# Performance work log

Measured on AMD Instinct MI355X. Metric: run time of the kernel, lower is better.

The kernel has to match this reference:

```python
import jax, jax.numpy as jnp
import numpy as np

B, T, C = 4, 2048, 1024
N_HEAD = 16
HEAD = C // N_HEAD

def setup_inputs() -> dict:
    key = jax.random.key(0)
    k1, k2, k3 = jax.random.split(key, 3)
    x = jax.random.normal(k1, (B, T, C), dtype=jnp.float32)
    w_attn = jax.random.normal(k2, (C, 3 * C), dtype=jnp.float32) * (1.0 / np.sqrt(C))
    w_proj = jax.random.normal(k3, (C, C), dtype=jnp.float32) * (1.0 / np.sqrt(C))
    return {"x": x, "w_attn": w_attn, "w_proj": w_proj}

def reference(x, w_attn, w_proj):
    b, t, c = x.shape
    qkv = x @ w_attn  # [B,T,3C]
    q, k, v = jnp.split(qkv, 3, axis=-1)
    # [B,T,C] -> [B,H,T,D]
    def heads(z):
        return z.reshape(b, t, N_HEAD, HEAD).transpose(0, 2, 1, 3)
    q, k, v = heads(q), heads(k), heads(v)
    scale = 1.0 / np.sqrt(HEAD)
    att = jnp.einsum('bhqd,bhkd->bhqk', q, k) * scale  # [B,H,T,T]
    causal = jnp.tril(jnp.ones((t, t), dtype=bool))
    att = jnp.where(causal[None, None], att, -jnp.inf)
    att = jax.nn.softmax(att, axis=-1)
    y = jnp.einsum('bhqk,bhkd->bhqd', att, v)  # [B,H,T,D]
    y = y.transpose(0, 2, 1, 3).reshape(b, t, c)
    return y @ w_proj
```

## Files before the change

kernel.cpp:

```cpp
#include <hip/hip_runtime.h>
#include <hip/hip_bf16.h>


typedef __attribute__((ext_vector_type(8))) short bf16x8;
typedef __attribute__((ext_vector_type(4))) float f32x4;

#define T_DIM 2048
#define NHEAD 16
#define HDIM  64

__device__ __forceinline__ unsigned short f2bf(float f) {
    union { float f; unsigned int u; } v; v.f = f;
    unsigned int r = v.u + 0x7fffu + ((v.u >> 16) & 1u);
    return (unsigned short)(r >> 16);
}

__device__ __forceinline__ void gload_lds16(const void* g, void* l) {
    __builtin_amdgcn_global_load_lds(
        (const __attribute__((address_space(1))) void*)g,
        (__attribute__((address_space(3))) void*)l,
        16, 0, 0);
}

__global__ void cvt_bf16_k(const float* __restrict__ src, unsigned short* __restrict__ dst, int n) {
    int i = (blockIdx.x * blockDim.x + threadIdx.x) * 4;
    if (i < n) {
        float4 v = *(const float4*)(src + i);
        ushort4 o; o.x = f2bf(v.x); o.y = f2bf(v.y); o.z = f2bf(v.z); o.w = f2bf(v.w);
        *(ushort4*)(dst + i) = o;
    }
}

__global__ void transpose_wb_k(const float* __restrict__ src, unsigned short* __restrict__ dst,
                               int R, int Cc) {
    __shared__ float tile[32][33];
    int c0 = blockIdx.x * 32, r0 = blockIdx.y * 32;
    int tx = threadIdx.x & 31, ty = threadIdx.x >> 5;
    #pragma unroll
    for (int i = 0; i < 32; i += 8)
        tile[ty + i][tx] = src[(size_t)(r0 + ty + i) * Cc + c0 + tx];
    __syncthreads();
    #pragma unroll
    for (int i = 0; i < 32; i += 8)
        dst[(size_t)(c0 + ty + i) * R + r0 + tx] = f2bf(tile[tx][ty + i]);
}

__global__ __launch_bounds__(256) void transpose_v_k(const unsigned short* __restrict__ vb,
                                                     unsigned short* __restrict__ vt) {
    __shared__ __align__(16) unsigned short L[64 * 72];
    const int bh = blockIdx.y, t0 = blockIdx.x * 64;
    const int tid = threadIdx.x;
    const unsigned short* src = vb + ((size_t)bh * T_DIM + t0) * HDIM;
    #pragma unroll
    for (int i = 0; i < 2; ++i) {
        int cc = tid + i * 256;
        int r = cc >> 3, g = cc & 7;
        *(uint4*)&L[r * 72 + g * 8] = *(const uint4*)(src + r * 64 + g * 8);
    }
    __syncthreads();
    unsigned short* dst = vt + (size_t)bh * HDIM * T_DIM + t0;
    #pragma unroll
    for (int i = 0; i < 2; ++i) {
        int cc = tid + i * 256;
        int d = cc >> 3, gt = cc & 7;
        unsigned short tmp[8];
        #pragma unroll
        for (int j = 0; j < 8; ++j) tmp[j] = L[(gt * 8 + j) * 72 + d];
        *(uint4*)(dst + (size_t)d * T_DIM + gt * 8) = *(uint4*)tmp;
    }
}

template<int EPI>
__global__ __launch_bounds__(512, 2) void gemm_bt_k(
    const unsigned short* __restrict__ A, const unsigned short* __restrict__ Bt,
    void* __restrict__ out0, void* __restrict__ out1, void* __restrict__ out2,
    int M, int N, int K)
{
    extern __shared__ __align__(16) unsigned short smem[];
    unsigned short* sA = smem;
    unsigned short* sB = smem + 49152;

    const int tid = threadIdx.x, lane = tid & 63, wave = tid >> 6;
    const int wm = wave >> 1, wn = wave & 1;
    const int lrow = lane & 15, hi = lane >> 4;

    const int nwg = gridDim.x * gridDim.y;
    const int lin = blockIdx.y * gridDim.x + blockIdx.x;
    const int lin2 = (lin & 7) * (nwg >> 3) + (lin >> 3);
    const int bxg = lin2 % gridDim.x, byg = lin2 / gridDim.x;
    const int row0 = byg * 256, col0 = bxg * 128;

    const int arow = tid >> 3;
    const int gk = ((tid & 7) ^ (arow & 7)) * 8;
    const unsigned short* gA0 = A + (size_t)(row0 + arow) * K + gk;
    const unsigned short* gA1 = A + (size_t)(row0 + arow + 64) * K + gk;
    const unsigned short* gA2 = A + (size_t)(row0 + arow + 128) * K + gk;
    const unsigned short* gA3 = A + (size_t)(row0 + arow + 192) * K + gk;
    const unsigned short* gB0 = Bt + (size_t)(col0 + arow) * K + gk;
    const unsigned short* gB1 = Bt + (size_t)(col0 + arow + 64) * K + gk;

    const int NT = K >> 6;

#define STAGE(ts, sl) { const size_t ko_ = (size_t)(ts) * 64; \
        unsigned short* dA_ = sA + (sl) * 16384; \
        unsigned short* dB_ = sB + (sl) * 8192; \
        gload_lds16(gA0 + ko_, dA_ + tid * 8); \
        gload_lds16(gA1 + ko_, dA_ + (tid + 512) * 8); \
        gload_lds16(gA2 + ko_, dA_ + (tid + 1024) * 8); \
        gload_lds16(gA3 + ko_, dA_ + (tid + 1536) * 8); \
        gload_lds16(gB0 + ko_, dB_ + tid * 8); \
        gload_lds16(gB1 + ko_, dB_ + (tid + 512) * 8); }

    f32x4 acc[4][4] = {};

    STAGE(0, 0);
    STAGE(1, 1);
    asm volatile("s_waitcnt vmcnt(6)" ::: "memory");
    __builtin_amdgcn_s_barrier();
    __builtin_amdgcn_sched_barrier(0);

    int slot = 0;
    for (int t = 0; t < NT; ++t) {
        if (t + 2 < NT) {
            const int s2 = (slot + 2 >= 3) ? slot - 1 : slot + 2;
            STAGE(t + 2, s2);
        }
        const unsigned short* As = sA + slot * 16384;
        const unsigned short* Bs = sB + slot * 8192;
        bf16x8 af[2][4], bf_[2][4];
        #pragma unroll
        for (int ks = 0; ks < 2; ++ks) {
            const int kc = (ks * 4 + hi) ^ (lrow & 7);
            #pragma unroll
            for (int mi = 0; mi < 4; ++mi)
                af[ks][mi] = *(const bf16x8*)&As[((wm * 64 + mi * 16 + lrow) * 8 + kc) * 8];
            #pragma unroll
            for (int ni = 0; ni < 4; ++ni)
                bf_[ks][ni] = *(const bf16x8*)&Bs[((wn * 64 + ni * 16 + lrow) * 8 + kc) * 8];
        }
        __builtin_amdgcn_s_setprio(1);
        #pragma unroll
        for (int ks = 0; ks < 2; ++ks)
            #pragma unroll
            for (int mi = 0; mi < 4; ++mi)
                #pragma unroll
                for (int ni = 0; ni < 4; ++ni)
                    acc[mi][ni] = __builtin_amdgcn_mfma_f32_16x16x32_bf16(af[ks][mi], bf_[ks][ni], acc[mi][ni], 0, 0, 0);
        __builtin_amdgcn_s_setprio(0);
        if (t + 2 < NT) { asm volatile("s_waitcnt vmcnt(6)" ::: "memory"); }
        else           { asm volatile("s_waitcnt vmcnt(0)" ::: "memory"); }
        __builtin_amdgcn_s_barrier();
        __builtin_amdgcn_sched_barrier(0);
        slot = (slot + 1 >= 3) ? 0 : slot + 1;
    }
#undef STAGE

    #pragma unroll
    for (int mi = 0; mi < 4; ++mi) {
        #pragma unroll
        for (int ni = 0; ni < 4; ++ni) {
            int gm0 = row0 + wm * 64 + mi * 16 + hi * 4;
            int gn  = col0 + wn * 64 + ni * 16 + lrow;
            #pragma unroll
            for (int r = 0; r < 4; ++r) {
                int gm = gm0 + r;
                float v = acc[mi][ni][r];
                if (EPI == 0) {
                    int which = gn >> 10, rem = gn & 1023;
                    int h = rem >> 6, d = rem & 63;
                    int bb = gm >> 11, t = gm & 2047;
                    if (which == 0) v *= 0.18033688011112042f;
                    unsigned short* dst = (unsigned short*)(which == 0 ? out0 : (which == 1 ? out1 : out2));
                    dst[((size_t)(bb * NHEAD + h) * T_DIM + t) * HDIM + d] = f2bf(v);
                } else {
                    ((float*)out0)[(size_t)gm * N + gn] = v;
                }
            }
        }
    }
}

__global__ __launch_bounds__(512) void attn_k(
    const unsigned short* __restrict__ qb, const unsigned short* __restrict__ kb,
    const unsigned short* __restrict__ vtb, unsigned short* __restrict__ yb)
{
    __shared__ __align__(16) unsigned short Ks[2][64 * 64];
    __shared__ __align__(16) unsigned short Vts[2][64 * 64];
    __shared__ __align__(16) unsigned short Ps[8][16 * 72];

    const int tid = threadIdx.x, lane = tid & 63, wave = tid >> 6;
    const int bh = blockIdx.y;
    const int lrow = lane & 15, hi = lane >> 4, lk = hi * 8;
    const unsigned short* Kg  = kb  + (size_t)bh * T_DIM * HDIM;
    const unsigned short* Vtg = vtb + (size_t)bh * HDIM * T_DIM;

    const int c = wave * 64 + lane;
    const int srow = c >> 3;
    const int sgp  = (c & 7) ^ (srow & 7);
    const size_t koff = (size_t)srow * 64 + sgp * 8;
    const size_t voff = (size_t)srow * T_DIM + sgp * 8;

    bf16x8 bones;
    #pragma unroll
    for (int j = 0; j < 8; ++j) bones[j] = (lrow == 0) ? (short)0x3F80 : (short)0;

    #pragma unroll
    for (int pass = 0; pass < 2; ++pass) {
        const int bx = (pass == 0) ? (int)blockIdx.x : (15 - (int)blockIdx.x);
        const int q0 = bx * 128;
        const int jtmax = 2 * bx + 1;
        const int wrow0 = q0 + wave * 16;

        const unsigned short* qrow = qb + ((size_t)bh * T_DIM + wrow0 + lrow) * HDIM;
        bf16x8 aq0 = *(const bf16x8*)(qrow + lk);
        bf16x8 aq1 = *(const bf16x8*)(qrow + 32 + lk);

        f32x4 o[4] = {};
        f32x4 ls = {};

        gload_lds16(Kg + koff, &Ks[0][wave * 512]);
        gload_lds16(Vtg + voff, &Vts[0][wave * 512]);
        __syncthreads();

        int cur = 0;
        for (int jt = 0; jt <= jtmax; ++jt) {
            if (jt < jtmax) {
                gload_lds16(Kg + (size_t)(jt + 1) * 64 * HDIM + koff, &Ks[cur ^ 1][wave * 512]);
                gload_lds16(Vtg + (size_t)(jt + 1) * 64 + voff, &Vts[cur ^ 1][wave * 512]);
            }
            if (jt * 64 <= wrow0 + 15) {
                f32x4 s[4] = {};
                #pragma unroll
                for (int kk = 0; kk < 2; ++kk) {
                    bf16x8 aq = kk ? aq1 : aq0;
                    #pragma unroll
                    for (int n = 0; n < 4; ++n) {
                        const int row = n * 16 + lrow;
                        const int gc = (kk * 4 + hi) ^ (lrow & 7);
                        bf16x8 bk = *(const bf16x8*)&Ks[cur][row * 64 + gc * 8];
                        s[n] = __builtin_amdgcn_mfma_f32_16x16x32_bf16(aq, bk, s[n], 0, 0, 0);
                    }
                }
                const int rbase = wrow0 + hi * 4;
                if (jt * 64 + 63 > wrow0) {
                    #pragma unroll
                    for (int n = 0; n < 4; ++n) {
                        const int kvcol = jt * 64 + n * 16 + lrow;
                        #pragma unroll
                        for (int r = 0; r < 4; ++r)
                            if (kvcol > rbase + r) s[n][r] = -1e30f;
                    }
                }
                #pragma unroll
                for (int n = 0; n < 4; ++n)
                    #pragma unroll
                    for (int r = 0; r < 4; ++r) {
                        float p = __builtin_amdgcn_exp2f(s[n][r] - 16.0f);
                        Ps[wave][(hi * 4 + r) * 72 + n * 16 + lrow] = f2bf(p);
                    }
                #pragma unroll
                for (int kk = 0; kk < 2; ++kk) {
                    bf16x8 pa = *(const bf16x8*)&Ps[wave][lrow * 72 + kk * 32 + lk];
                    #pragma unroll
                    for (int dn = 0; dn < 4; ++dn) {
                        const int row = dn * 16 + lrow;
                        const int gc = (kk * 4 + hi) ^ (lrow & 7);
                        bf16x8 bv = *(const bf16x8*)&Vts[cur][row * 64 + gc * 8];
                        o[dn] = __builtin_amdgcn_mfma_f32_16x16x32_bf16(pa, bv, o[dn], 0, 0, 0);
                    }
                    ls = __builtin_amdgcn_mfma_f32_16x16x32_bf16(pa, bones, ls, 0, 0, 0);
                }
            }
            __syncthreads();
            cur ^= 1;
        }

        const int bb = bh >> 4, h = bh & 15;
        #pragma unroll
        for (int r = 0; r < 4; ++r) {
            float lsum = __shfl(ls[r], lane & 48);
            float inv = 1.0f / lsum;
            int t = q0 + wave * 16 + hi * 4 + r;
            size_t rowoff = ((size_t)(bb * T_DIM + t)) * 1024 + h * HDIM;
            #pragma unroll
            for (int dn = 0; dn < 4; ++dn)
                yb[rowoff + dn * 16 + lrow] = f2bf(o[dn][r] * inv);
        }
    }
}

extern "C" void kernel_launch(void* const* d_in, const int* in_sizes, int n_in,
                              void* d_out, int out_size, void* d_ws, size_t ws_size,
                              hipStream_t stream) {
    const float* x      = (const float*)d_in[0];
    const float* w_attn = (const float*)d_in[1];
    const float* w_proj = (const float*)d_in[2];
    float* out = (float*)d_out;

    unsigned short* xb  = (unsigned short*)d_ws;
    unsigned short* wat = xb  + (size_t)8192 * 1024;
    unsigned short* wpt = wat + (size_t)3072 * 1024;
    unsigned short* qb  = wpt + (size_t)1024 * 1024;
    unsigned short* kb  = qb  + (size_t)64 * 2048 * 64;
    unsigned short* vb  = kb  + (size_t)64 * 2048 * 64;
    unsigned short* yb  = vb  + (size_t)64 * 2048 * 64;
    unsigned short* vt  = xb;

    (void)hipFuncSetAttribute((const void*)gemm_bt_k<0>,
                              hipFuncAttributeMaxDynamicSharedMemorySize, 147456);
    (void)hipFuncSetAttribute((const void*)gemm_bt_k<1>,
                              hipFuncAttributeMaxDynamicSharedMemorySize, 147456);

    cvt_bf16_k<<<8192, 256, 0, stream>>>(x, xb, 8192 * 1024);
    transpose_wb_k<<<dim3(96, 32), 256, 0, stream>>>(w_attn, wat, 1024, 3072);
    transpose_wb_k<<<dim3(32, 32), 256, 0, stream>>>(w_proj, wpt, 1024, 1024);

    gemm_bt_k<0><<<dim3(24, 32), 512, 147456, stream>>>(xb, wat, qb, kb, vb, 8192, 3072, 1024);
    transpose_v_k<<<dim3(32, 64), 256, 0, stream>>>(vb, vt);
    attn_k<<<dim3(8, 64), 512, 0, stream>>>(qb, kb, vt, yb);
    gemm_bt_k<1><<<dim3(8, 32), 512, 147456, stream>>>(yb, wpt, out, nullptr, nullptr, 8192, 1024, 1024);
}
```

Before: 184.0 us.

## Rewrite attention with 32x32 MFMA, register P, and fragment-ordered K/V layout

The QKV GEMM epilogue now writes K and V straight into tile-blocked, MFMA-fragment-ordered layouts, so the separate V transpose kernel is dropped. The attention kernel switches to 32x32x16 MFMA computing S^T with K as the A operand. P is kept in registers via cvt_pk_bf16 and permlane32_swap instead of a round trip through LDS, and the row sum is taken with scalar adds rather than a ones-MFMA. Each block now handles 256 query rows per pass, which halves the grid to 4x64 blocks and may lower occupancy and load balance.

```diff
diff --git a/kernel.cpp b/kernel.cpp
--- a/kernel.cpp
+++ b/kernel.cpp
@@ -4,6 +4,7 @@
 
 typedef __attribute__((ext_vector_type(8))) short bf16x8;
 typedef __attribute__((ext_vector_type(4))) float f32x4;
+typedef __attribute__((ext_vector_type(16))) float f32x16;
 
 #define T_DIM 2048
 #define NHEAD 16
@@ -13,6 +14,20 @@
     union { float f; unsigned int u; } v; v.f = f;
     unsigned int r = v.u + 0x7fffu + ((v.u >> 16) & 1u);
     return (unsigned short)(r >> 16);
+}
+
+__device__ __forceinline__ unsigned cvtpk_bf16(float lo, float hi) {
+    unsigned r;
+    asm("v_cvt_pk_bf16_f32 %0, %1, %2" : "=v"(r) : "v"(lo), "v"(hi));
+    return r;
+}
+__device__ __forceinline__ void pl32swap(unsigned &x, unsigned &y) {
+    asm("v_permlane32_swap_b32 %0, %1" : "+v"(x), "+v"(y));
+}
+__device__ __forceinline__ bf16x8 mk8(unsigned w0, unsigned w1, unsigned w2, unsigned w3) {
+    union { unsigned u[4]; bf16x8 v; } p;
+    p.u[0] = w0; p.u[1] = w1; p.u[2] = w2; p.u[3] = w3;
+    return p.v;
 }
 
 __device__ __forceinline__ void gload_lds16(const void* g, void* l) {
@@ -43,31 +58,6 @@
     #pragma unroll
     for (int i = 0; i < 32; i += 8)
         dst[(size_t)(c0 + ty + i) * R + r0 + tx] = f2bf(tile[tx][ty + i]);
-}
-
-__global__ __launch_bounds__(256) void transpose_v_k(const unsigned short* __restrict__ vb,
-                                                     unsigned short* __restrict__ vt) {
-    __shared__ __align__(16) unsigned short L[64 * 72];
-    const int bh = blockIdx.y, t0 = blockIdx.x * 64;
-    const int tid = threadIdx.x;
-    const unsigned short* src = vb + ((size_t)bh * T_DIM + t0) * HDIM;
-    #pragma unroll
-    for (int i = 0; i < 2; ++i) {
-        int cc = tid + i * 256;
-        int r = cc >> 3, g = cc & 7;
-        *(uint4*)&L[r * 72 + g * 8] = *(const uint4*)(src + r * 64 + g * 8);
-    }
-    __syncthreads();
-    unsigned short* dst = vt + (size_t)bh * HDIM * T_DIM + t0;
-    #pragma unroll
-    for (int i = 0; i < 2; ++i) {
-        int cc = tid + i * 256;
-        int d = cc >> 3, gt = cc & 7;
-        unsigned short tmp[8];
-        #pragma unroll
-        for (int j = 0; j < 8; ++j) tmp[j] = L[(gt * 8 + j) * 72 + d];
-        *(uint4*)(dst + (size_t)d * T_DIM + gt * 8) = *(uint4*)tmp;
-    }
 }
 
 template<int EPI>
@@ -169,9 +159,17 @@
                     int which = gn >> 10, rem = gn & 1023;
                     int h = rem >> 6, d = rem & 63;
                     int bb = gm >> 11, t = gm & 2047;
-                    if (which == 0) v *= 0.18033688011112042f;
-                    unsigned short* dst = (unsigned short*)(which == 0 ? out0 : (which == 1 ? out1 : out2));
-                    dst[((size_t)(bb * NHEAD + h) * T_DIM + t) * HDIM + d] = f2bf(v);
+                    int bh = bb * NHEAD + h;
+                    if (which == 0) {
+                        ((unsigned short*)out0)[((size_t)bh * T_DIM + t) * HDIM + d] =
+                            f2bf(v * 0.18033688011112042f);
+                    } else if (which == 1) {
+                        ((unsigned short*)out1)[(size_t)(bh * 32 + (t >> 6)) * 4096 +
+                            (size_t)((d >> 3) * 64 + (t & 63)) * 8 + (d & 7)] = f2bf(v);
+                    } else {
+                        ((unsigned short*)out2)[(size_t)(bh * 32 + (t >> 6)) * 4096 +
+                            (size_t)(((t >> 3) & 7) * 64 + d) * 8 + (t & 7)] = f2bf(v);
+                    }
                 } else {
                     ((float*)out0)[(size_t)gm * N + gn] = v;
                 }
@@ -181,110 +179,104 @@
 }
 
 __global__ __launch_bounds__(512) void attn_k(
-    const unsigned short* __restrict__ qb, const unsigned short* __restrict__ kb,
-    const unsigned short* __restrict__ vtb, unsigned short* __restrict__ yb)
+    const unsigned short* __restrict__ qb, const unsigned short* __restrict__ kcm,
+    const unsigned short* __restrict__ vcm, unsigned short* __restrict__ yb)
 {
-    __shared__ __align__(16) unsigned short Ks[2][64 * 64];
-    __shared__ __align__(16) unsigned short Vts[2][64 * 64];
-    __shared__ __align__(16) unsigned short Ps[8][16 * 72];
+    __shared__ __align__(16) unsigned short Ks[2][4096];
+    __shared__ __align__(16) unsigned short Vs[2][4096];
 
     const int tid = threadIdx.x, lane = tid & 63, wave = tid >> 6;
     const int bh = blockIdx.y;
-    const int lrow = lane & 15, hi = lane >> 4, lk = hi * 8;
-    const unsigned short* Kg  = kb  + (size_t)bh * T_DIM * HDIM;
-    const unsigned short* Vtg = vtb + (size_t)bh * HDIM * T_DIM;
-
-    const int c = wave * 64 + lane;
-    const int srow = c >> 3;
-    const int sgp  = (c & 7) ^ (srow & 7);
-    const size_t koff = (size_t)srow * 64 + sgp * 8;
-    const size_t voff = (size_t)srow * T_DIM + sgp * 8;
-
-    bf16x8 bones;
-    #pragma unroll
-    for (int j = 0; j < 8; ++j) bones[j] = (lrow == 0) ? (short)0x3F80 : (short)0;
+    const int q32 = lane & 31, hi32 = lane >> 5;
+    const unsigned short* Kg = kcm + (size_t)bh * 32 * 4096;
+    const unsigned short* Vg = vcm + (size_t)bh * 32 * 4096;
 
     #pragma unroll
     for (int pass = 0; pass < 2; ++pass) {
-        const int bx = (pass == 0) ? (int)blockIdx.x : (15 - (int)blockIdx.x);
-        const int q0 = bx * 128;
-        const int jtmax = 2 * bx + 1;
-        const int wrow0 = q0 + wave * 16;
-
-        const unsigned short* qrow = qb + ((size_t)bh * T_DIM + wrow0 + lrow) * HDIM;
-        bf16x8 aq0 = *(const bf16x8*)(qrow + lk);
-        bf16x8 aq1 = *(const bf16x8*)(qrow + 32 + lk);
-
-        f32x4 o[4] = {};
-        f32x4 ls = {};
-
-        gload_lds16(Kg + koff, &Ks[0][wave * 512]);
-        gload_lds16(Vtg + voff, &Vts[0][wave * 512]);
+        const int bxx = (pass == 0) ? (int)blockIdx.x : (7 - (int)blockIdx.x);
+        const int ntiles = 4 * bxx + 4;
+        const int q0w = bxx * 256 + wave * 32;
+        const int qg = q0w + q32;
+
+        const unsigned short* qrow = qb + ((size_t)bh * T_DIM + q0w + q32) * HDIM;
+        bf16x8 qf[4];
+        #pragma unroll
+        for (int kc = 0; kc < 4; ++kc)
+            qf[kc] = *(const bf16x8*)(qrow + kc * 16 + hi32 * 8);
+
+        f32x16 o0 = {}, o1 = {};
+        float lsum = 0.f;
+
+        gload_lds16(Kg + tid * 8, &Ks[0][tid * 8]);
+        gload_lds16(Vg + tid * 8, &Vs[0][tid * 8]);
         __syncthreads();
 
         int cur = 0;
-        for (int jt = 0; jt <= jtmax; ++jt) {
-            if (jt < jtmax) {
-                gload_lds16(Kg + (size_t)(jt + 1) * 64 * HDIM + koff, &Ks[cur ^ 1][wave * 512]);
-                gload_lds16(Vtg + (size_t)(jt + 1) * 64 + voff, &Vts[cur ^ 1][wave * 512]);
+        for (int jt = 0; jt < ntiles; ++jt) {
+            if (jt + 1 < ntiles) {
+                gload_lds16(Kg + (size_t)(jt + 1) * 4096 + tid * 8, &Ks[cur ^ 1][tid * 8]);
+                gload_lds16(Vg + (size_t)(jt + 1) * 4096 + tid * 8, &Vs[cur ^ 1][tid * 8]);
             }
-            if (jt * 64 <= wrow0 + 15) {
-                f32x4 s[4] = {};
+            if (jt * 64 <= q0w + 31) {
+                f32x16 s0 = {}, s1 = {};
                 #pragma unroll
-                for (int kk = 0; kk < 2; ++kk) {
-                    bf16x8 aq = kk ? aq1 : aq0;
+                for (int kc = 0; kc < 4; ++kc) {
+                    bf16x8 a0 = *(const bf16x8*)&Ks[cur][((kc * 2 + hi32) * 64 + q32) * 8];
+                    bf16x8 a1 = *(const bf16x8*)&Ks[cur][((kc * 2 + hi32) * 64 + 32 + q32) * 8];
+                    s0 = __builtin_amdgcn_mfma_f32_32x32x16_bf16(a0, qf[kc], s0, 0, 0, 0);
+                    s1 = __builtin_amdgcn_mfma_f32_32x32x16_bf16(a1, qf[kc], s1, 0, 0, 0);
+                }
+                if (jt * 64 + 63 > q0w) {
                     #pragma unroll
-                    for (int n = 0; n < 4; ++n) {
-                        const int row = n * 16 + lrow;
-                        const int gc = (kk * 4 + hi) ^ (lrow & 7);
-                        bf16x8 bk = *(const bf16x8*)&Ks[cur][row * 64 + gc * 8];
-                        s[n] = __builtin_amdgcn_mfma_f32_16x16x32_bf16(aq, bk, s[n], 0, 0, 0);
+                    for (int r = 0; r < 16; ++r) {
+                        int kv0 = jt * 64 + (r & 3) + 8 * (r >> 2) + 4 * hi32;
+                        if (kv0 > qg)      s0[r] = -1e30f;
+                        if (kv0 + 32 > qg) s1[r] = -1e30f;
                     }
                 }
-                const int rbase = wrow0 + hi * 4;
-                if (jt * 64 + 63 > wrow0) {
+                bf16x8 pa[4];
+                #pragma unroll
+                for (int blk = 0; blk < 2; ++blk) {
+                    float p_[16]; unsigned w_[8];
                     #pragma unroll
-                    for (int n = 0; n < 4; ++n) {
-                        const int kvcol = jt * 64 + n * 16 + lrow;
-                        #pragma unroll
-                        for (int r = 0; r < 4; ++r)
-                            if (kvcol > rbase + r) s[n][r] = -1e30f;
+                    for (int i = 0; i < 16; ++i) {
+                        float sv = blk ? s1[i] : s0[i];
+                        p_[i] = __builtin_amdgcn_exp2f(sv - 16.0f);
+                        lsum += p_[i];
                     }
+                    #pragma unroll
+                    for (int i = 0; i < 8; ++i) w_[i] = cvtpk_bf16(p_[2 * i], p_[2 * i + 1]);
+                    pl32swap(w_[0], w_[2]); pl32swap(w_[1], w_[3]);
+                    pl32swap(w_[4], w_[6]); pl32swap(w_[5], w_[7]);
+                    pa[blk * 2]     = mk8(w_[0], w_[1], w_[2], w_[3]);
+                    pa[blk * 2 + 1] = mk8(w_[4], w_[5], w_[6], w_[7]);
                 }
                 #pragma unroll
-                for (int n = 0; n < 4; ++n)
-                    #pragma unroll
-                    for (int r = 0; r < 4; ++r) {
-                        float p = __builtin_amdgcn_exp2f(s[n][r] - 16.0f);
-                        Ps[wave][(hi * 4 + r) * 72 + n * 16 + lrow] = f2bf(p);
-                    }
-                #pragma unroll
-                for (int kk = 0; kk < 2; ++kk) {
-                    bf16x8 pa = *(const bf16x8*)&Ps[wave][lrow * 72 + kk * 32 + lk];
-                    #pragma unroll
-                    for (int dn = 0; dn < 4; ++dn) {
-                        const int row = dn * 16 + lrow;
-                        const int gc = (kk * 4 + hi) ^ (lrow & 7);
-                        bf16x8 bv = *(const bf16x8*)&Vts[cur][row * 64 + gc * 8];
-                        o[dn] = __builtin_amdgcn_mfma_f32_16x16x32_bf16(pa, bv, o[dn], 0, 0, 0);
-                    }
-                    ls = __builtin_amdgcn_mfma_f32_16x16x32_bf16(pa, bones, ls, 0, 0, 0);
+                for (int kvc = 0; kvc < 4; ++kvc) {
+                    bf16x8 b0 = *(const bf16x8*)&Vs[cur][((kvc * 2 + hi32) * 64 + q32) * 8];
+                    bf16x8 b1 = *(const bf16x8*)&Vs[cur][((kvc * 2 + hi32) * 64 + 32 + q32) * 8];
+                    o0 = __builtin_amdgcn_mfma_f32_32x32x16_bf16(pa[kvc], b0, o0, 0, 0, 0);
+                    o1 = __builtin_amdgcn_mfma_f32_32x32x16_bf16(pa[kvc], b1, o1, 0, 0, 0);
                 }
             }
             __syncthreads();
             cur ^= 1;
         }
 
-        const int bb = bh >> 4, h = bh & 15;
-        #pragma unroll
-        for (int r = 0; r < 4; ++r) {
-            float lsum = __shfl(ls[r], lane & 48);
-            float inv = 1.0f / lsum;
-            int t = q0 + wave * 16 + hi * 4 + r;
-            size_t rowoff = ((size_t)(bb * T_DIM + t)) * 1024 + h * HDIM;
-            #pragma unroll
-            for (int dn = 0; dn < 4; ++dn)
-                yb[rowoff + dn * 16 + lrow] = f2bf(o[dn][r] * inv);
+        {
+            unsigned la = __float_as_uint(lsum), lb = __float_as_uint(lsum);
+            pl32swap(la, lb);
+            lsum = __uint_as_float(la) + __uint_as_float(lb);
+        }
+        const int bb2 = bh >> 4, h = bh & 15;
+        #pragma unroll
+        for (int r = 0; r < 16; ++r) {
+            const int cr = (r & 3) + 8 * (r >> 2) + 4 * hi32;
+            float inv = 1.0f / __shfl(lsum, cr);
+            int t = q0w + cr;
+            size_t off = ((size_t)(bb2 * T_DIM + t)) * 1024 + h * HDIM + q32;
+            yb[off]      = f2bf(o0[r] * inv);
+            yb[off + 32] = f2bf(o1[r] * inv);
         }
     }
 }
@@ -301,10 +293,9 @@
     unsigned short* wat = xb  + (size_t)8192 * 1024;
     unsigned short* wpt = wat + (size_t)3072 * 1024;
     unsigned short* qb  = wpt + (size_t)1024 * 1024;
-    unsigned short* kb  = qb  + (size_t)64 * 2048 * 64;
-    unsigned short* vb  = kb  + (size_t)64 * 2048 * 64;
-    unsigned short* yb  = vb  + (size_t)64 * 2048 * 64;
-    unsigned short* vt  = xb;
+    unsigned short* kcm = qb  + (size_t)64 * 2048 * 64;
+    unsigned short* vcm = kcm + (size_t)64 * 2048 * 64;
+    unsigned short* yb  = vcm + (size_t)64 * 2048 * 64;
 
     (void)hipFuncSetAttribute((const void*)gemm_bt_k<0>,
                               hipFuncAttributeMaxDynamicSharedMemorySize, 147456);
@@ -315,8 +306,7 @@
     transpose_wb_k<<<dim3(96, 32), 256, 0, stream>>>(w_attn, wat, 1024, 3072);
     transpose_wb_k<<<dim3(32, 32), 256, 0, stream>>>(w_proj, wpt, 1024, 1024);
 
-    gemm_bt_k<0><<<dim3(24, 32), 512, 147456, stream>>>(xb, wat, qb, kb, vb, 8192, 3072, 1024);
-    transpose_v_k<<<dim3(32, 64), 256, 0, stream>>>(vb, vt);
-    attn_k<<<dim3(8, 64), 512, 0, stream>>>(qb, kb, vt, yb);
+    gemm_bt_k<0><<<dim3(24, 32), 512, 147456, stream>>>(xb, wat, qb, kcm, vcm, 8192, 3072, 1024);
+    attn_k<<<dim3(4, 64), 512, 0, stream>>>(qb, kcm, vcm, yb);
     gemm_bt_k<1><<<dim3(8, 32), 512, 147456, stream>>>(yb, wpt, out, nullptr, nullptr, 8192, 1024, 1024);
 }
```

Result: faster. 172.5 us (-6.2%).
